# Optimization experiments

Measured on AMD Instinct MI355X. Metric: run time of the kernel, lower is better.

Reference implementation:

```python
import jax, jax.numpy as jnp
import numpy as np
import math

TAU_PLUS = 20.0
TAU_MINUS = 20.0
A_PLUS = 0.01
A_MINUS = 0.01
W_MAX = 1.0
W_MIN = 0.0
TARGET_RATE = 0.1
HOMEO = 0.001
RATE_ALPHA = 0.01
DT = 1.0


def setup_inputs() -> dict:
    key = jax.random.key(0)
    k1, k2, k3, k4 = jax.random.split(key, 4)
    B, PRE, POST = 1024, 4096, 4096
    return {
        "pre_spikes": jax.random.uniform(k1, (B, PRE), dtype=jnp.float32),
        "post_spikes": jax.random.uniform(k2, (B, POST), dtype=jnp.float32),
        "weights": jax.random.uniform(k3, (POST, PRE), dtype=jnp.float32) * 0.5,
        "pre_trace": jnp.zeros((B, PRE), dtype=jnp.float32),
        "post_trace": jnp.zeros((B, POST), dtype=jnp.float32),
        "running_rate": jax.random.uniform(k4, (POST,), dtype=jnp.float32) * 0.2,
    }


def reference(pre_spikes, post_spikes, weights, pre_trace, post_trace, running_rate):
    B = pre_spikes.shape[0]
    # trace decay
    pre_tr = pre_trace * math.exp(-DT / TAU_PLUS)
    post_tr = post_trace * math.exp(-DT / TAU_MINUS)
    # STDP weight update (learn=True, auto_scale=False)
    dw_plus = A_PLUS * jnp.einsum('bp,bq->pq', post_spikes, pre_tr) / B
    dw_minus = -A_MINUS * jnp.einsum('bp,bq->pq', post_tr, pre_spikes) / B
    dw_homeo = -HOMEO * (running_rate - TARGET_RATE)[:, None]
    new_weights = jnp.clip(weights + dw_plus + dw_minus + dw_homeo, W_MIN, W_MAX)
    # homeostatic rate EMA
    batch_rate = post_spikes.mean(axis=0)
    new_rate = running_rate * (1.0 - RATE_ALPHA) + RATE_ALPHA * batch_rate
    # trace update
    new_pre_trace = pre_tr + pre_spikes
    new_post_trace = post_tr + post_spikes
    # postsynaptic current with updated weights
    current = pre_spikes @ new_weights.T  # (B, POST)
    return current, new_weights, new_pre_trace, new_post_trace, new_rate
```

## Files before the change

### kernel.cpp

```cpp
#include <hip/hip_runtime.h>
#include <hip/hip_fp8.h>

typedef __attribute__((ext_vector_type(8))) short short8;
typedef __attribute__((ext_vector_type(4))) float floatx4;
typedef __attribute__((ext_vector_type(8))) int int8v;
typedef __attribute__((ext_vector_type(4))) int int4v;

#define LDS_PTR(x) ((__attribute__((address_space(3))) unsigned int*)(x))
#define GLB_PTR(x) ((const __attribute__((address_space(1))) unsigned int*)(x))

__device__ __forceinline__ unsigned short f2bf(float f) {
    unsigned int u = __float_as_uint(f);
    unsigned int r = (u + 0x7FFFu + ((u >> 16) & 1u)) >> 16;
    return (unsigned short)r;
}
__device__ __forceinline__ unsigned char f2fp8(float f) {
    __hip_fp8_e4m3 v(f);
    return (unsigned char)v.__x;
}
__device__ __forceinline__ float fp82f(unsigned int u) {
    __hip_fp8_e4m3 v;
    v.__x = (__hip_fp8_storage_t)(u & 0xFF);
    return (float)v;
}

__global__ __launch_bounds__(256) void prep_post_kernel(
    const float* __restrict__ S, const float* __restrict__ T,
    float* __restrict__ traceOut, unsigned char* __restrict__ At,
    int C, int K2, int Bsz, float dp)
{
    __shared__ float sT[64][65];
    __shared__ float tT[64][65];
    const int t = threadIdx.x;
    const int r0 = blockIdx.y * 64, c0 = blockIdx.x * 64;
#pragma unroll
    for (int i = 0; i < 4; ++i) {
        int rl = (t >> 4) + i * 16;
        int cl = (t & 15) * 4;
        size_t g = (size_t)(r0 + rl) * C + c0 + cl;
        float4 s4 = *(const float4*)&S[g];
        float4 t4 = *(const float4*)&T[g];
        float4 o;
        o.x = fmaf(t4.x, dp, s4.x); o.y = fmaf(t4.y, dp, s4.y);
        o.z = fmaf(t4.z, dp, s4.z); o.w = fmaf(t4.w, dp, s4.w);
        *(float4*)&traceOut[g] = o;
        sT[rl][cl + 0] = s4.x; sT[rl][cl + 1] = s4.y;
        sT[rl][cl + 2] = s4.z; sT[rl][cl + 3] = s4.w;
        tT[rl][cl + 0] = t4.x; tT[rl][cl + 1] = t4.y;
        tT[rl][cl + 2] = t4.z; tT[rl][cl + 3] = t4.w;
    }
    __syncthreads();
#pragma unroll
    for (int i = 0; i < 4; ++i) {
        int cl = (t >> 4) + i * 16;
        int rl = (t & 15) * 4;
        uchar4 a, b;
        a.x = f2fp8(sT[rl + 0][cl]); a.y = f2fp8(sT[rl + 1][cl]);
        a.z = f2fp8(sT[rl + 2][cl]); a.w = f2fp8(sT[rl + 3][cl]);
        b.x = f2fp8(tT[rl + 0][cl]); b.y = f2fp8(tT[rl + 1][cl]);
        b.z = f2fp8(tT[rl + 2][cl]); b.w = f2fp8(tT[rl + 3][cl]);
        *(uchar4*)&At[(size_t)(c0 + cl) * K2 + r0 + rl] = a;
        *(uchar4*)&At[(size_t)(c0 + cl) * K2 + Bsz + r0 + rl] = b;
    }
}

__global__ __launch_bounds__(256) void prep_pre_kernel(
    const float* __restrict__ S, const float* __restrict__ T,
    float* __restrict__ traceOut, unsigned char* __restrict__ Bt,
    unsigned short* __restrict__ preBf,
    int C, int K2, int Bsz, float dp)
{
    __shared__ float sT[64][65];
    __shared__ float tT[64][65];
    const int t = threadIdx.x;
    const int r0 = blockIdx.y * 64, c0 = blockIdx.x * 64;
#pragma unroll
    for (int i = 0; i < 4; ++i) {
        int rl = (t >> 4) + i * 16;
        int cl = (t & 15) * 4;
        size_t g = (size_t)(r0 + rl) * C + c0 + cl;
        float4 s4 = *(const float4*)&S[g];
        float4 t4 = *(const float4*)&T[g];
        float4 o;
        o.x = fmaf(t4.x, dp, s4.x); o.y = fmaf(t4.y, dp, s4.y);
        o.z = fmaf(t4.z, dp, s4.z); o.w = fmaf(t4.w, dp, s4.w);
        *(float4*)&traceOut[g] = o;
        ushort4 pb = { f2bf(s4.x), f2bf(s4.y), f2bf(s4.z), f2bf(s4.w) };
        *(ushort4*)&preBf[g] = pb;
        sT[rl][cl + 0] = s4.x; sT[rl][cl + 1] = s4.y;
        sT[rl][cl + 2] = s4.z; sT[rl][cl + 3] = s4.w;
        tT[rl][cl + 0] = t4.x; tT[rl][cl + 1] = t4.y;
        tT[rl][cl + 2] = t4.z; tT[rl][cl + 3] = t4.w;
    }
    __syncthreads();
#pragma unroll
    for (int i = 0; i < 4; ++i) {
        int cl = (t >> 4) + i * 16;
        int rl = (t & 15) * 4;
        uchar4 a, b;
        a.x = f2fp8(tT[rl + 0][cl]); a.y = f2fp8(tT[rl + 1][cl]);
        a.z = f2fp8(tT[rl + 2][cl]); a.w = f2fp8(tT[rl + 3][cl]);
        b.x = f2fp8(-sT[rl + 0][cl]); b.y = f2fp8(-sT[rl + 1][cl]);
        b.z = f2fp8(-sT[rl + 2][cl]); b.w = f2fp8(-sT[rl + 3][cl]);
        *(uchar4*)&Bt[(size_t)(c0 + cl) * K2 + r0 + rl] = a;
        *(uchar4*)&Bt[(size_t)(c0 + cl) * K2 + Bsz + r0 + rl] = b;
    }
}

__global__ __launch_bounds__(256) void rate_kernel(
    const unsigned char* __restrict__ At, const float* __restrict__ rr,
    float* __restrict__ new_rate, int K2, int Bsz)
{
    const int w = threadIdx.x >> 6, l = threadIdx.x & 63;
    const int p = blockIdx.x * 4 + w;
    const unsigned char* row = At + (size_t)p * K2;
    float s = 0.f;
    for (int k = l * 16; k < Bsz; k += 1024) {
        int4v v = *(const int4v*)&row[k];
#pragma unroll
        for (int wd = 0; wd < 4; ++wd) {
            unsigned int u = (unsigned int)v[wd];
            s += fp82f(u) + fp82f(u >> 8) + fp82f(u >> 16) + fp82f(u >> 24);
        }
    }
#pragma unroll
    for (int off = 32; off > 0; off >>= 1) s += __shfl_xor(s, off, 64);
    if (l == 0)
        new_rate[p] = rr[p] * 0.99f + 0.01f * (s / (float)Bsz);
}

__global__ __launch_bounds__(256) void dw_fp8_kernel(
    const unsigned char* __restrict__ A, const unsigned char* __restrict__ B,
    int K, int N, float s,
    const float* __restrict__ Wold, const float* __restrict__ rr,
    float* __restrict__ outF, unsigned short* __restrict__ outBf)
{
    constexpr int BM = 128, BN = 128, BK = 128;
    __shared__ unsigned char lA[BM * BK];
    __shared__ unsigned char lB[BN * BK];

    const int t = threadIdx.x;
    const int l = t & 63;
    const int w = t >> 6;
    const int wm = w >> 1, wn = w & 1;
    const int bm = blockIdx.y, bn = blockIdx.x;

    floatx4 acc[4][4] = {};

    for (int k0 = 0; k0 < K; k0 += BK) {
#pragma unroll
        for (int i = 0; i < 4; ++i) {
            int ci = i * 256 + t;
            int r = ci >> 3, sc = ci & 7;
            int g = sc ^ (r & 7);
            const unsigned char* gpA = A + (size_t)(bm * BM + r) * K + k0 + g * 16;
            __builtin_amdgcn_global_load_lds(GLB_PTR(gpA),
                LDS_PTR(&lA[ci * 16]), 16, 0, 0);
            const unsigned char* gpB = B + (size_t)(bn * BN + r) * K + k0 + g * 16;
            __builtin_amdgcn_global_load_lds(GLB_PTR(gpB),
                LDS_PTR(&lB[ci * 16]), 16, 0, 0);
        }
        __syncthreads();

        const int c = l >> 4;
        const int m = l & 15;
        int8v af[4], bf[4];
#pragma unroll
        for (int i = 0; i < 4; ++i) {
            int ra = wm * 64 + i * 16 + m;
            int s0 = (2 * c) ^ (ra & 7), s1 = (2 * c + 1) ^ (ra & 7);
            int4v lo = *(const int4v*)&lA[ra * BK + s0 * 16];
            int4v hi = *(const int4v*)&lA[ra * BK + s1 * 16];
            af[i][0] = lo[0]; af[i][1] = lo[1]; af[i][2] = lo[2]; af[i][3] = lo[3];
            af[i][4] = hi[0]; af[i][5] = hi[1]; af[i][6] = hi[2]; af[i][7] = hi[3];
        }
#pragma unroll
        for (int j = 0; j < 4; ++j) {
            int rb = wn * 64 + j * 16 + m;
            int s0 = (2 * c) ^ (rb & 7), s1 = (2 * c + 1) ^ (rb & 7);
            int4v lo = *(const int4v*)&lB[rb * BK + s0 * 16];
            int4v hi = *(const int4v*)&lB[rb * BK + s1 * 16];
            bf[j][0] = lo[0]; bf[j][1] = lo[1]; bf[j][2] = lo[2]; bf[j][3] = lo[3];
            bf[j][4] = hi[0]; bf[j][5] = hi[1]; bf[j][6] = hi[2]; bf[j][7] = hi[3];
        }
#pragma unroll
        for (int i = 0; i < 4; ++i)
#pragma unroll
            for (int j = 0; j < 4; ++j)
                acc[i][j] = __builtin_amdgcn_mfma_scale_f32_16x16x128_f8f6f4(
                    af[i], bf[j], acc[i][j], 0, 0, 0, 0x7f, 0, 0x7f);
        __syncthreads();
    }

    const int pBase = bm * BM + wm * 64;
    const int qBase = bn * BN + wn * 64;
#pragma unroll
    for (int i = 0; i < 4; ++i) {
#pragma unroll
        for (int r = 0; r < 4; ++r) {
            const int p = pBase + i * 16 + (l >> 4) * 4 + r;
            const float hp = -0.001f * (rr[p] - 0.1f);
#pragma unroll
            for (int j = 0; j < 4; ++j) {
                const int q = qBase + j * 16 + (l & 15);
                const size_t idx = (size_t)p * N + q;
                float v = fmaf(s, acc[i][j][r], Wold[idx] + hp);
                v = fminf(fmaxf(v, 0.f), 1.f);
                outF[idx] = v;
                outBf[idx] = f2bf(v);
            }
        }
    }
}

template <int BM, int BN>
__global__ __launch_bounds__(256) void mfma_gemm_bt(
    const unsigned short* __restrict__ A,
    const unsigned short* __restrict__ Bm,
    int K, int N, float* __restrict__ outF)
{
    constexpr int BK = 32;
    constexpr int FI = BM / 32;
    constexpr int FJ = BN / 32;
    __shared__ unsigned short lA[BM * BK];
    __shared__ unsigned short lB[BN * BK];

    const int t = threadIdx.x;
    const int l = t & 63;
    const int w = t >> 6;
    const int wm = w >> 1, wn = w & 1;
    const int bm = blockIdx.y, bn = blockIdx.x;

    const int srow = t >> 2;
    const int sc = t & 3;
    const int gc = sc ^ ((srow >> 1) & 3);
    const int skc = sc * 8;
    const int gkc = gc * 8;

    floatx4 acc[FI][FJ] = {};

    for (int k0 = 0; k0 < K; k0 += BK) {
#pragma unroll
        for (int i = 0; i < BM / 64; ++i) {
            const unsigned short* gp =
                A + (size_t)(bm * BM + i * 64 + srow) * K + k0 + gkc;
            __builtin_amdgcn_global_load_lds(GLB_PTR(gp),
                LDS_PTR(&lA[(i * 64 + srow) * BK + skc]), 16, 0, 0);
        }
#pragma unroll
        for (int i = 0; i < BN / 64; ++i) {
            const unsigned short* gp =
                Bm + (size_t)(bn * BN + i * 64 + srow) * K + k0 + gkc;
            __builtin_amdgcn_global_load_lds(GLB_PTR(gp),
                LDS_PTR(&lB[(i * 64 + srow) * BK + skc]), 16, 0, 0);
        }
        __syncthreads();

        const int q = l >> 4;
        short8 af[FI], bf[FJ];
#pragma unroll
        for (int i = 0; i < FI; ++i) {
            int ra = wm * (BM / 2) + i * 16 + (l & 15);
            af[i] = *(const short8*)&lA[ra * BK + ((q ^ ((ra >> 1) & 3)) * 8)];
        }
#pragma unroll
        for (int j = 0; j < FJ; ++j) {
            int rb = wn * (BN / 2) + j * 16 + (l & 15);
            bf[j] = *(const short8*)&lB[rb * BK + ((q ^ ((rb >> 1) & 3)) * 8)];
        }
#pragma unroll
        for (int i = 0; i < FI; ++i)
#pragma unroll
            for (int j = 0; j < FJ; ++j)
                acc[i][j] = __builtin_amdgcn_mfma_f32_16x16x32_bf16(
                    af[i], bf[j], acc[i][j], 0, 0, 0);
        __syncthreads();
    }

    const int pBase = bm * BM + wm * (BM / 2);
    const int qBase = bn * BN + wn * (BN / 2);
#pragma unroll
    for (int i = 0; i < FI; ++i)
#pragma unroll
        for (int r = 0; r < 4; ++r) {
            const int p = pBase + i * 16 + (l >> 4) * 4 + r;
#pragma unroll
            for (int j = 0; j < FJ; ++j) {
                const int q = qBase + j * 16 + (l & 15);
                outF[(size_t)p * N + q] = acc[i][j][r];
            }
        }
}

extern "C" void kernel_launch(void* const* d_in, const int* in_sizes, int n_in,
                              void* d_out, int out_size, void* d_ws, size_t ws_size,
                              hipStream_t stream)
{
    const float* pre_spikes   = (const float*)d_in[0];
    const float* post_spikes  = (const float*)d_in[1];
    const float* weights      = (const float*)d_in[2];
    const float* pre_trace    = (const float*)d_in[3];
    const float* post_trace   = (const float*)d_in[4];
    const float* running_rate = (const float*)d_in[5];

    const int POST = in_sizes[5];
    const int PRE  = in_sizes[2] / POST;
    const int Bsz  = in_sizes[0] / PRE;
    const int K2   = 2 * Bsz;

    const size_t nCur   = (size_t)Bsz * POST;
    const size_t nW     = (size_t)POST * PRE;
    const size_t nPreT  = (size_t)Bsz * PRE;
    const size_t nPostT = (size_t)Bsz * POST;

    float* out_current    = (float*)d_out;
    float* out_weights    = out_current + nCur;
    float* out_pre_trace  = out_weights + nW;
    float* out_post_trace = out_pre_trace + nPreT;
    float* out_rate       = out_post_trace + nPostT;

    unsigned char* At     = (unsigned char*)d_ws;
    unsigned char* Bt     = At + (size_t)POST * K2;
    unsigned short* preBf = (unsigned short*)(Bt + (size_t)PRE * K2);
    unsigned short* wBf   = preBf + nPreT;

    const float dp = 0.95122942450071400910f;
    const float s  = dp * (0.01f / (float)Bsz);

    prep_post_kernel<<<dim3(POST / 64, Bsz / 64), 256, 0, stream>>>(
        post_spikes, post_trace, out_post_trace, At, POST, K2, Bsz, dp);
    prep_pre_kernel<<<dim3(PRE / 64, Bsz / 64), 256, 0, stream>>>(
        pre_spikes, pre_trace, out_pre_trace, Bt, preBf, PRE, K2, Bsz, dp);

    rate_kernel<<<POST / 4, 256, 0, stream>>>(
        At, running_rate, out_rate, K2, Bsz);

    dw_fp8_kernel<<<dim3(PRE / 128, POST / 128), 256, 0, stream>>>(
        At, Bt, K2, PRE, s, weights, running_rate, out_weights, wBf);

    mfma_gemm_bt<64, 128><<<dim3(POST / 128, Bsz / 64), 256, 0, stream>>>(
        preBf, wBf, PRE, POST, out_current);
}
```

Before: 345.0 us.

## Double-buffer LDS tiles in fp8 dW and bf16 GEMM kernels

Both GEMM kernels now keep two LDS buffers and prefetch the next K tile with global_load_lds while MFMAs run on the current one. This is meant to hide global-to-LDS load latency behind compute. Shared memory use doubles, to 64KB in the fp8 kernel, which may lower occupancy. Each iteration now waits on vmcnt(0) plus a raw barrier instead of __syncthreads.

```diff
diff --git a/kernel.cpp b/kernel.cpp
--- a/kernel.cpp
+++ b/kernel.cpp
@@ -136,8 +136,8 @@
     float* __restrict__ outF, unsigned short* __restrict__ outBf)
 {
     constexpr int BM = 128, BN = 128, BK = 128;
-    __shared__ unsigned char lA[BM * BK];
-    __shared__ unsigned char lB[BN * BK];
+    __shared__ unsigned char lA[2][BM * BK];
+    __shared__ unsigned char lB[2][BN * BK];
 
     const int t = threadIdx.x;
     const int l = t & 63;
@@ -147,7 +147,7 @@
 
     floatx4 acc[4][4] = {};
 
-    for (int k0 = 0; k0 < K; k0 += BK) {
+    auto stage = [&](int buf, int k0) {
 #pragma unroll
         for (int i = 0; i < 4; ++i) {
             int ci = i * 256 + t;
@@ -155,12 +155,20 @@
             int g = sc ^ (r & 7);
             const unsigned char* gpA = A + (size_t)(bm * BM + r) * K + k0 + g * 16;
             __builtin_amdgcn_global_load_lds(GLB_PTR(gpA),
-                LDS_PTR(&lA[ci * 16]), 16, 0, 0);
+                LDS_PTR(&lA[buf][ci * 16]), 16, 0, 0);
             const unsigned char* gpB = B + (size_t)(bn * BN + r) * K + k0 + g * 16;
             __builtin_amdgcn_global_load_lds(GLB_PTR(gpB),
-                LDS_PTR(&lB[ci * 16]), 16, 0, 0);
-        }
-        __syncthreads();
+                LDS_PTR(&lB[buf][ci * 16]), 16, 0, 0);
+        }
+    };
+
+    stage(0, 0);
+    __syncthreads();
+
+    const int nT = K / BK;
+    int cur = 0;
+    for (int tt = 0; tt < nT; ++tt) {
+        if (tt + 1 < nT) stage(cur ^ 1, (tt + 1) * BK);
 
         const int c = l >> 4;
         const int m = l & 15;
@@ -169,8 +177,8 @@
         for (int i = 0; i < 4; ++i) {
             int ra = wm * 64 + i * 16 + m;
             int s0 = (2 * c) ^ (ra & 7), s1 = (2 * c + 1) ^ (ra & 7);
-            int4v lo = *(const int4v*)&lA[ra * BK + s0 * 16];
-            int4v hi = *(const int4v*)&lA[ra * BK + s1 * 16];
+            int4v lo = *(const int4v*)&lA[cur][ra * BK + s0 * 16];
+            int4v hi = *(const int4v*)&lA[cur][ra * BK + s1 * 16];
             af[i][0] = lo[0]; af[i][1] = lo[1]; af[i][2] = lo[2]; af[i][3] = lo[3];
             af[i][4] = hi[0]; af[i][5] = hi[1]; af[i][6] = hi[2]; af[i][7] = hi[3];
         }
@@ -178,8 +186,8 @@
         for (int j = 0; j < 4; ++j) {
             int rb = wn * 64 + j * 16 + m;
             int s0 = (2 * c) ^ (rb & 7), s1 = (2 * c + 1) ^ (rb & 7);
-            int4v lo = *(const int4v*)&lB[rb * BK + s0 * 16];
-            int4v hi = *(const int4v*)&lB[rb * BK + s1 * 16];
+            int4v lo = *(const int4v*)&lB[cur][rb * BK + s0 * 16];
+            int4v hi = *(const int4v*)&lB[cur][rb * BK + s1 * 16];
             bf[j][0] = lo[0]; bf[j][1] = lo[1]; bf[j][2] = lo[2]; bf[j][3] = lo[3];
             bf[j][4] = hi[0]; bf[j][5] = hi[1]; bf[j][6] = hi[2]; bf[j][7] = hi[3];
         }
@@ -189,7 +197,10 @@
             for (int j = 0; j < 4; ++j)
                 acc[i][j] = __builtin_amdgcn_mfma_scale_f32_16x16x128_f8f6f4(
                     af[i], bf[j], acc[i][j], 0, 0, 0, 0x7f, 0, 0x7f);
-        __syncthreads();
+
+        asm volatile("s_waitcnt vmcnt(0)" ::: "memory");
+        __builtin_amdgcn_s_barrier();
+        cur ^= 1;
     }
 
     const int pBase = bm * BM + wm * 64;
@@ -222,8 +233,8 @@
     constexpr int BK = 32;
     constexpr int FI = BM / 32;
     constexpr int FJ = BN / 32;
-    __shared__ unsigned short lA[BM * BK];
-    __shared__ unsigned short lB[BN * BK];
+    __shared__ unsigned short lA[2][BM * BK];
+    __shared__ unsigned short lB[2][BN * BK];
 
     const int t = threadIdx.x;
     const int l = t & 63;
@@ -239,34 +250,42 @@
 
     floatx4 acc[FI][FJ] = {};
 
-    for (int k0 = 0; k0 < K; k0 += BK) {
+    auto stage = [&](int buf, int k0) {
 #pragma unroll
         for (int i = 0; i < BM / 64; ++i) {
             const unsigned short* gp =
                 A + (size_t)(bm * BM + i * 64 + srow) * K + k0 + gkc;
             __builtin_amdgcn_global_load_lds(GLB_PTR(gp),
-                LDS_PTR(&lA[(i * 64 + srow) * BK + skc]), 16, 0, 0);
+                LDS_PTR(&lA[buf][(i * 64 + srow) * BK + skc]), 16, 0, 0);
         }
 #pragma unroll
         for (int i = 0; i < BN / 64; ++i) {
             const unsigned short* gp =
                 Bm + (size_t)(bn * BN + i * 64 + srow) * K + k0 + gkc;
             __builtin_amdgcn_global_load_lds(GLB_PTR(gp),
-                LDS_PTR(&lB[(i * 64 + srow) * BK + skc]), 16, 0, 0);
-        }
-        __syncthreads();
+                LDS_PTR(&lB[buf][(i * 64 + srow) * BK + skc]), 16, 0, 0);
+        }
+    };
+
+    stage(0, 0);
+    __syncthreads();
+
+    const int nT = K / BK;
+    int cur = 0;
+    for (int tt = 0; tt < nT; ++tt) {
+        if (tt + 1 < nT) stage(cur ^ 1, (tt + 1) * BK);
 
         const int q = l >> 4;
         short8 af[FI], bf[FJ];
 #pragma unroll
         for (int i = 0; i < FI; ++i) {
             int ra = wm * (BM / 2) + i * 16 + (l & 15);
-            af[i] = *(const short8*)&lA[ra * BK + ((q ^ ((ra >> 1) & 3)) * 8)];
+            af[i] = *(const short8*)&lA[cur][ra * BK + ((q ^ ((ra >> 1) & 3)) * 8)];
         }
 #pragma unroll
         for (int j = 0; j < FJ; ++j) {
             int rb = wn * (BN / 2) + j * 16 + (l & 15);
-            bf[j] = *(const short8*)&lB[rb * BK + ((q ^ ((rb >> 1) & 3)) * 8)];
+            bf[j] = *(const short8*)&lB[cur][rb * BK + ((q ^ ((rb >> 1) & 3)) * 8)];
         }
 #pragma unroll
         for (int i = 0; i < FI; ++i)
@@ -274,7 +293,10 @@
             for (int j = 0; j < FJ; ++j)
                 acc[i][j] = __builtin_amdgcn_mfma_f32_16x16x32_bf16(
                     af[i], bf[j], acc[i][j], 0, 0, 0);
-        __syncthreads();
+
+        asm volatile("s_waitcnt vmcnt(0)" ::: "memory");
+        __builtin_amdgcn_s_barrier();
+        cur ^= 1;
     }
 
     const int pBase = bm * BM + wm * (BM / 2);
```

Result: faster. 336.4 us (-2.5%).
